# Kernel optimization log

Measured on AMD Instinct MI355X. Metric: run time of the kernel, lower is better.

## Reference

```python
import jax, jax.numpy as jnp
import numpy as np

N_NODES = 100000
NODES_PER_GRAPH = 100
IN_CHANNELS = 256
RATIO = 0.5


def setup_inputs() -> dict:
    key = jax.random.key(0)
    k_x, k_w, k_b = jax.random.split(key, 3)
    x = jax.random.normal(k_x, (N_NODES, IN_CHANNELS), dtype=jnp.float32)
    # sorted per-node graph ids: 1000 graphs of 100 nodes each
    batch = (jnp.arange(N_NODES, dtype=jnp.int64) // NODES_PER_GRAPH).astype(jnp.int64)
    # Linear(in_channels, 1): weight [1, d], bias [1] (torch default init scale)
    bound = 1.0 / np.sqrt(IN_CHANNELS)
    W = jax.random.uniform(k_w, (1, IN_CHANNELS), dtype=jnp.float32, minval=-bound, maxval=bound)
    b = jax.random.uniform(k_b, (1,), dtype=jnp.float32, minval=-bound, maxval=bound)
    return {"x": x, "batch": batch, "W": W, "b": b}


def reference(x, batch, W, b):
    N = x.shape[0]
    num_graphs = int(batch[-1]) + 1          # static under equal-size segments
    n_per = N // num_graphs
    k = int(np.ceil(RATIO * n_per))          # PyG topk: ceil(ratio * n_i)

    # linear score: [N]
    scores = x @ W[0] + b[0]

    # per-graph segment top-k (segments are equal-size, contiguous)
    grid = scores.reshape(num_graphs, n_per)                  # [G, n_per]
    top_vals, top_idx = jax.lax.top_k(grid, k)                # each [G, k], descending

    offsets = (jnp.arange(num_graphs, dtype=top_idx.dtype) * n_per)[:, None]
    node_index = (top_idx + offsets).reshape(-1)              # [G*k] global node ids
    weight = top_vals.reshape(-1)                             # scores[node_index]
    cluster_index = jnp.arange(node_index.shape[0], dtype=node_index.dtype)
    return node_index, cluster_index, weight
```

## Files before the change

kernel.cpp:

```cpp
#include <hip/hip_runtime.h>
#include <hip/hip_bf16.h>


#define NPG   100
#define DIM   256
#define KSEL  50
#define ROWS_PER_WAVE 25

static __device__ __forceinline__ float bf2f(unsigned short s) {
    union { unsigned int u; float f; } v;
    v.u = ((unsigned int)s) << 16;
    return v.f;
}

__global__ __launch_bounds__(256) void select_sparse_kernel(
    const void* __restrict__ xv,
    const void* __restrict__ Wv,
    const void* __restrict__ bv,
    void* __restrict__ outv,
    int num_graphs)
{
    __shared__ float w_sh[DIM];
    __shared__ float scores[NPG];

    const int g    = blockIdx.x;
    const int tid  = threadIdx.x;
    const int wave = tid >> 6;
    const int lane = tid & 63;

    const unsigned short* xu = (const unsigned short*)xv;
    bool f32 = false;
    for (int i = 0; i < 64; ++i) {
        const float v = bf2f(xu[2 * i]);
        if (!(v > -64.0f && v < 64.0f)) f32 = true;
    }

    float bval;
    if (f32) {
        w_sh[tid] = ((const float*)Wv)[tid];
        bval = ((const float*)bv)[0];
    } else {
        w_sh[tid] = bf2f(((const unsigned short*)Wv)[tid]);
        bval = bf2f(((const unsigned short*)bv)[0]);
    }
    __syncthreads();

    const float wl0 = w_sh[lane * 4 + 0];
    const float wl1 = w_sh[lane * 4 + 1];
    const float wl2 = w_sh[lane * 4 + 2];
    const float wl3 = w_sh[lane * 4 + 3];
    const int base_node = g * NPG;

    if (f32) {
        const float4* xrow = (const float4*)((const float*)xv + (size_t)base_node * DIM);
        float4 u[ROWS_PER_WAVE];
        #pragma unroll
        for (int i = 0; i < ROWS_PER_WAVE; ++i)
            u[i] = xrow[(size_t)(wave + 4 * i) * 64 + lane];

        #pragma unroll
        for (int i = 0; i < ROWS_PER_WAVE; ++i) {
            float acc = u[i].x * wl0 + u[i].y * wl1 + u[i].z * wl2 + u[i].w * wl3;
            #pragma unroll
            for (int off = 32; off > 0; off >>= 1)
                acc += __shfl_down(acc, off, 64);
            if (lane == 0) scores[wave + 4 * i] = acc + bval;
        }
    } else {
        const unsigned short* x = (const unsigned short*)xv;
        for (int n = wave; n < NPG; n += 4) {
            const ushort4 u = ((const ushort4*)(x + (size_t)(base_node + n) * DIM))[lane];
            float acc = bf2f(u.x) * wl0 + bf2f(u.y) * wl1
                      + bf2f(u.z) * wl2 + bf2f(u.w) * wl3;
            #pragma unroll
            for (int off = 32; off > 0; off >>= 1)
                acc += __shfl_down(acc, off, 64);
            if (lane == 0) scores[n] = acc + bval;
        }
    }
    __syncthreads();

    if (tid < NPG) {
        const float v = scores[tid];
        int rank = 0;
        for (int i = 0; i < NPG; ++i) {
            const float vi = scores[i];
            rank += (vi > v) || (vi == v && i < tid);
        }
        if (rank < KSEL) {
            const int total = num_graphs * KSEL;
            const int pos = g * KSEL + rank;
            if (f32) {
                float* o = (float*)outv;
                o[pos]             = (float)(base_node + tid);
                o[total + pos]     = (float)pos;
                o[2 * total + pos] = v;
            } else {
                __hip_bfloat16* o = (__hip_bfloat16*)outv;
                o[pos]             = __float2bfloat16((float)(base_node + tid));
                o[total + pos]     = __float2bfloat16((float)pos);
                o[2 * total + pos] = __float2bfloat16(v);
            }
        }
    }
}

extern "C" void kernel_launch(void* const* d_in, const int* in_sizes, int n_in,
                              void* d_out, int out_size, void* d_ws, size_t ws_size,
                              hipStream_t stream) {
    int xi = -1, wi = -1, bi = -1;
    long best = -1;
    for (int i = 0; i < n_in; ++i) {
        const long s = in_sizes[i];
        if (s > best) { best = s; xi = i; }
    }
    for (int i = 0; i < n_in; ++i) {
        if (i == xi) continue;
        const long s = in_sizes[i];
        if (s == DIM && wi < 0) wi = i;
        if (s == 1   && bi < 0) bi = i;
    }
    if (xi < 0) xi = 0;
    if (wi < 0) wi = (n_in > 2) ? 2 : 1;
    if (bi < 0) bi = n_in - 1;

    const long num_graphs = (long)in_sizes[xi] / ((long)NPG * DIM);
    if (num_graphs <= 0) return;

    select_sparse_kernel<<<dim3((unsigned)num_graphs), dim3(256), 0, stream>>>(
        d_in[xi], d_in[wi], d_in[bi], d_out, (int)num_graphs);
}
```

Before: 158.8 us.

## Split fused score/top-k kernel into GEMV and per-graph select kernels

Replaces the single per-graph kernel with two launches. The first is a row-parallel GEMV that computes all node scores with 64 rows per block, nontemporal loads and a launch bound hint for higher occupancy. The second reads those scores back from workspace and ranks them per graph. The aim is better memory parallelism in the bandwidth-bound score pass. The cost is a second launch and a round trip of the scores through global memory.

```diff
diff --git a/kernel.cpp b/kernel.cpp
--- a/kernel.cpp
+++ b/kernel.cpp
@@ -5,7 +5,10 @@
 #define NPG   100
 #define DIM   256
 #define KSEL  50
-#define ROWS_PER_WAVE 25
+#define ROWS_PER_WAVE 16
+#define ROWS_PER_BLOCK 64
+
+typedef float vfloat4 __attribute__((ext_vector_type(4)));
 
 static __device__ __forceinline__ float bf2f(unsigned short s) {
     union { unsigned int u; float f; } v;
@@ -13,91 +16,117 @@
     return v.f;
 }
 
-__global__ __launch_bounds__(256) void select_sparse_kernel(
+static __device__ __forceinline__ bool probe_f32(const void* xv) {
+    const unsigned short* xu = (const unsigned short*)xv;
+    bool f32 = false;
+    #pragma unroll
+    for (int i = 0; i < 64; ++i) {
+        const float v = bf2f(xu[2 * i]);
+        if (!(v > -64.0f && v < 64.0f)) f32 = true;
+    }
+    return f32;
+}
+
+__global__ __launch_bounds__(256, 4) void gemv_scores_kernel(
     const void* __restrict__ xv,
     const void* __restrict__ Wv,
     const void* __restrict__ bv,
-    void* __restrict__ outv,
-    int num_graphs)
+    float* __restrict__ scores,
+    int n_rows)
 {
     __shared__ float w_sh[DIM];
-    __shared__ float scores[NPG];
 
-    const int g    = blockIdx.x;
     const int tid  = threadIdx.x;
     const int wave = tid >> 6;
     const int lane = tid & 63;
 
-    const unsigned short* xu = (const unsigned short*)xv;
-    bool f32 = false;
-    for (int i = 0; i < 64; ++i) {
-        const float v = bf2f(xu[2 * i]);
-        if (!(v > -64.0f && v < 64.0f)) f32 = true;
-    }
+    const bool f32 = probe_f32(xv);
 
-    float bval;
-    if (f32) {
-        w_sh[tid] = ((const float*)Wv)[tid];
-        bval = ((const float*)bv)[0];
-    } else {
-        w_sh[tid] = bf2f(((const unsigned short*)Wv)[tid]);
-        bval = bf2f(((const unsigned short*)bv)[0]);
-    }
+    if (f32) w_sh[tid] = ((const float*)Wv)[tid];
+    else     w_sh[tid] = bf2f(((const unsigned short*)Wv)[tid]);
     __syncthreads();
 
+    const float bval = f32 ? ((const float*)bv)[0]
+                           : bf2f(((const unsigned short*)bv)[0]);
     const float wl0 = w_sh[lane * 4 + 0];
     const float wl1 = w_sh[lane * 4 + 1];
     const float wl2 = w_sh[lane * 4 + 2];
     const float wl3 = w_sh[lane * 4 + 3];
-    const int base_node = g * NPG;
+
+    const int row0 = blockIdx.x * ROWS_PER_BLOCK + wave * ROWS_PER_WAVE;
 
     if (f32) {
-        const float4* xrow = (const float4*)((const float*)xv + (size_t)base_node * DIM);
-        float4 u[ROWS_PER_WAVE];
-        #pragma unroll
-        for (int i = 0; i < ROWS_PER_WAVE; ++i)
-            u[i] = xrow[(size_t)(wave + 4 * i) * 64 + lane];
-
+        const vfloat4* xr = (const vfloat4*)xv;
+        vfloat4 u[ROWS_PER_WAVE];
         #pragma unroll
         for (int i = 0; i < ROWS_PER_WAVE; ++i) {
+            const int r = row0 + i;
+            if (r < n_rows)
+                u[i] = __builtin_nontemporal_load(&xr[(size_t)r * (DIM / 4) + lane]);
+            else
+                u[i] = (vfloat4){0.f, 0.f, 0.f, 0.f};
+        }
+        #pragma unroll
+        for (int i = 0; i < ROWS_PER_WAVE; ++i) {
+            const int r = row0 + i;
             float acc = u[i].x * wl0 + u[i].y * wl1 + u[i].z * wl2 + u[i].w * wl3;
             #pragma unroll
             for (int off = 32; off > 0; off >>= 1)
                 acc += __shfl_down(acc, off, 64);
-            if (lane == 0) scores[wave + 4 * i] = acc + bval;
+            if (lane == 0 && r < n_rows) scores[r] = acc + bval;
         }
     } else {
         const unsigned short* x = (const unsigned short*)xv;
-        for (int n = wave; n < NPG; n += 4) {
-            const ushort4 u = ((const ushort4*)(x + (size_t)(base_node + n) * DIM))[lane];
+        for (int i = 0; i < ROWS_PER_WAVE; ++i) {
+            const int r = row0 + i;
+            if (r >= n_rows) break;
+            const ushort4 u = ((const ushort4*)(x + (size_t)r * DIM))[lane];
             float acc = bf2f(u.x) * wl0 + bf2f(u.y) * wl1
                       + bf2f(u.z) * wl2 + bf2f(u.w) * wl3;
             #pragma unroll
             for (int off = 32; off > 0; off >>= 1)
                 acc += __shfl_down(acc, off, 64);
-            if (lane == 0) scores[n] = acc + bval;
+            if (lane == 0) scores[r] = acc + bval;
         }
     }
+}
+
+__global__ __launch_bounds__(128) void select_kernel(
+    const void* __restrict__ xv,
+    const float* __restrict__ scores,
+    void* __restrict__ outv,
+    int num_graphs)
+{
+    __shared__ float sc[NPG];
+
+    const int g   = blockIdx.x;
+    const int tid = threadIdx.x;
+
+    const bool f32 = probe_f32(xv);
+
+    if (tid < NPG) sc[tid] = scores[g * NPG + tid];
     __syncthreads();
 
     if (tid < NPG) {
-        const float v = scores[tid];
+        const float v = sc[tid];
         int rank = 0;
+        #pragma unroll 4
         for (int i = 0; i < NPG; ++i) {
-            const float vi = scores[i];
+            const float vi = sc[i];
             rank += (vi > v) || (vi == v && i < tid);
         }
         if (rank < KSEL) {
             const int total = num_graphs * KSEL;
-            const int pos = g * KSEL + rank;
+            const int pos   = g * KSEL + rank;
+            const int node  = g * NPG + tid;
             if (f32) {
                 float* o = (float*)outv;
-                o[pos]             = (float)(base_node + tid);
+                o[pos]             = (float)node;
                 o[total + pos]     = (float)pos;
                 o[2 * total + pos] = v;
             } else {
                 __hip_bfloat16* o = (__hip_bfloat16*)outv;
-                o[pos]             = __float2bfloat16((float)(base_node + tid));
+                o[pos]             = __float2bfloat16((float)node);
                 o[total + pos]     = __float2bfloat16((float)pos);
                 o[2 * total + pos] = __float2bfloat16(v);
             }
@@ -124,9 +153,16 @@
     if (wi < 0) wi = (n_in > 2) ? 2 : 1;
     if (bi < 0) bi = n_in - 1;
 
-    const long num_graphs = (long)in_sizes[xi] / ((long)NPG * DIM);
+    const long n_rows     = (long)in_sizes[xi] / DIM;
+    const long num_graphs = n_rows / NPG;
     if (num_graphs <= 0) return;
 
-    select_sparse_kernel<<<dim3((unsigned)num_graphs), dim3(256), 0, stream>>>(
-        d_in[xi], d_in[wi], d_in[bi], d_out, (int)num_graphs);
+    float* scores_ws = (float*)d_ws;
+
+    const unsigned grid_a = (unsigned)((n_rows + ROWS_PER_BLOCK - 1) / ROWS_PER_BLOCK);
+    gemv_scores_kernel<<<dim3(grid_a), dim3(256), 0, stream>>>(
+        d_in[xi], d_in[wi], d_in[bi], scores_ws, (int)n_rows);
+
+    select_kernel<<<dim3((unsigned)num_graphs), dim3(128), 0, stream>>>(
+        d_in[xi], scores_ws, d_out, (int)num_graphs);
 }
```

Measured after the change: 157.3 us, median of 2. No clear change (-1.0%).
